# Kernel tuning notes

Measured on AMD Instinct MI355X. Metric: run time of the kernel, lower is better.

The kernel has to match this reference:

```python
import math
import jax, jax.numpy as jnp
import numpy as np

S, B, H, D = 2048, 1, 16, 128  # seq, batch, heads, head_dim (hard-coded in source)
COEFF = 1.0  # layer_num = 1
NORM_FACTOR = math.sqrt(2048 / 16) * COEFF  # sqrt(HIDDEN/NUM_HEADS) * coeff


def setup_inputs() -> dict:
    key = jax.random.key(0)
    k1, k2, k3, k4, k5 = jax.random.split(key, 5)
    query_layer = jax.random.normal(k1, (S, B, H, D), dtype=jnp.float32)
    key_layer = jax.random.normal(k2, (S, B, H, D), dtype=jnp.float32)
    value_layer = jax.random.normal(k3, (S, B, H, D), dtype=jnp.float32)
    # causal mask, True = masked (Megatron convention)
    attention_mask = jnp.triu(jnp.ones((S, S), dtype=bool), k=1)[None, None]
    # per-head SVD right-singular-vector matrices (orthonormal-ish; random here)
    svd_qk = jax.random.normal(k4, (H, D, D), dtype=jnp.float32) / math.sqrt(D)
    svd_v = jax.random.normal(k5, (H, D, D), dtype=jnp.float32) / math.sqrt(D)
    return {"query_layer": query_layer, "key_layer": key_layer,
            "value_layer": value_layer, "attention_mask": attention_mask,
            "svd_qk": svd_qk, "svd_v": svd_v}


def reference(query_layer, key_layer, value_layer, attention_mask, svd_qk, svd_v):
    # q/k/v: [S, 1, H, D] -> project each head through its SVD matrix
    q = jnp.einsum('shd,hde->hse', query_layer[:, 0], svd_qk)  # [H,S,D]
    k = jnp.einsum('shd,hde->hse', key_layer[:, 0], svd_qk)    # [H,S,D]
    # qk_drop = 0 -> h_mask zeroing of columns is a no-op (faithfully skipped)
    scores = jnp.einsum('hqe,hke->hqk', q, k) / NORM_FACTOR    # [H,S,S]
    mask = attention_mask[0, 0]                                 # [S,S] bool
    scores = jnp.where(mask, jnp.float32(-10000.0), scores)
    # FusedScaleMaskSoftmax: scale by coeff, re-mask, softmax
    scaled = jnp.where(mask, jnp.float32(-10000.0), scores * COEFF)
    probs = jax.nn.softmax(scaled, axis=-1)                     # [H,S,S]
    # attention dropout is identity in eval mode
    v = jnp.einsum('shd,hde->hse', value_layer[:, 0], svd_v)    # [H,S,D]
    # vlinear_drop = 0 -> column zeroing is a no-op
    ctx = jnp.einsum('hqk,hke->qhe', probs, v)                  # [S,H,D]
    return ctx.reshape(S, B, H * D)                             # [S,1,2048]
```

## Files before the change

### kernel.cpp

```cpp
#include <hip/hip_runtime.h>
#include <hip/hip_bf16.h>
#include <math.h>

#define S_LEN 2048
#define NHEAD 16
#define DHEAD 128

typedef __attribute__((ext_vector_type(8)))  _Float16 f16x8;
typedef __attribute__((ext_vector_type(4)))  _Float16 f16x4;
typedef __attribute__((ext_vector_type(4)))  float    f32x4;
typedef __attribute__((ext_vector_type(16))) float    f32x16;

__device__ __forceinline__ void permswap(unsigned &a, unsigned &b) {
    asm volatile("v_permlane32_swap_b32 %0, %1" : "+v"(a), "+v"(b));
}

typedef __attribute__((address_space(3))) unsigned int lds_u32;
typedef __attribute__((address_space(1))) const unsigned int glb_u32;
__device__ __forceinline__ void gload16(const void* g, void* l) {
    __builtin_amdgcn_global_load_lds((glb_u32*)g, (lds_u32*)l, 16, 0, 0);
}

__global__ __launch_bounds__(256) void transpose_w_kernel(
    const float* __restrict__ w_qk, const float* __restrict__ w_v,
    _Float16* __restrict__ wqk_t, _Float16* __restrict__ wv_t)
{
    __shared__ float tile[32][33];
    const int mat = blockIdx.z;
    const int h   = blockIdx.y;
    const int t0  = blockIdx.x;
    const int dt  = (t0 >> 2) * 32;
    const int et  = (t0 & 3) * 32;
    const float* src = (mat ? w_v : w_qk) + (size_t)h * DHEAD * DHEAD;
    _Float16*   dst = (mat ? wv_t : wqk_t) + (size_t)h * DHEAD * DHEAD;
    const int tx = threadIdx.x & 31, ty = threadIdx.x >> 5;
#pragma unroll
    for (int k = 0; k < 4; ++k)
        tile[ty + 8 * k][tx] = src[(size_t)(dt + ty + 8 * k) * DHEAD + et + tx];
    __syncthreads();
#pragma unroll
    for (int k = 0; k < 4; ++k)
        dst[(size_t)(et + ty + 8 * k) * DHEAD + dt + tx] = (_Float16)tile[tx][ty + 8 * k];
}

__global__ __launch_bounds__(256) void proj_kernel(
    const float* __restrict__ q_in, const float* __restrict__ k_in,
    const float* __restrict__ v_in,
    const _Float16* __restrict__ wqk_t, const _Float16* __restrict__ wv_t,
    _Float16* __restrict__ Qp, _Float16* __restrict__ Kp, _Float16* __restrict__ Vt)
{
    const int h   = blockIdx.x >> 5;
    const int rb  = blockIdx.x & 31;
    const int wv  = threadIdx.x >> 6;
    const int lane = threadIdx.x & 63;
    const int r16 = lane & 15;
    const int kg  = lane >> 4;
    const int s_base = rb * 64 + wv * 16;
    const int s_row  = s_base + r16;
    const float INV_NORM = 0.12752211758f;

    f16x8 aq[4], ak[4], av[4];
    {
        const float* qr = q_in + ((size_t)s_row * NHEAD + h) * DHEAD;
        const float* kr = k_in + ((size_t)s_row * NHEAD + h) * DHEAD;
        const float* vr = v_in + ((size_t)s_row * NHEAD + h) * DHEAD;
#pragma unroll
        for (int kb = 0; kb < 4; ++kb) {
            const int d0 = kb * 32 + kg * 8;
            const f32x4 q0 = *(const f32x4*)(qr + d0), q1 = *(const f32x4*)(qr + d0 + 4);
            const f32x4 k0 = *(const f32x4*)(kr + d0), k1 = *(const f32x4*)(kr + d0 + 4);
            const f32x4 v0 = *(const f32x4*)(vr + d0), v1 = *(const f32x4*)(vr + d0 + 4);
#pragma unroll
            for (int i = 0; i < 4; ++i) {
                aq[kb][i] = (_Float16)q0[i];  aq[kb][i + 4] = (_Float16)q1[i];
                ak[kb][i] = (_Float16)k0[i];  ak[kb][i + 4] = (_Float16)k1[i];
                av[kb][i] = (_Float16)v0[i];  av[kb][i + 4] = (_Float16)v1[i];
            }
        }
    }

    const _Float16* wq_h = wqk_t + (size_t)h * DHEAD * DHEAD;
    const _Float16* wv_h = wv_t  + (size_t)h * DHEAD * DHEAD;

#pragma unroll 2
    for (int cb = 0; cb < 8; ++cb) {
        f32x4 accq = {0.f, 0.f, 0.f, 0.f};
        f32x4 acck = {0.f, 0.f, 0.f, 0.f};
        f32x4 accv = {0.f, 0.f, 0.f, 0.f};
        const int c = cb * 16 + r16;
#pragma unroll
        for (int kb = 0; kb < 4; ++kb) {
            const f16x8 bqk = *(const f16x8*)(wq_h + (size_t)c * DHEAD + kb * 32 + kg * 8);
            const f16x8 bv  = *(const f16x8*)(wv_h + (size_t)c * DHEAD + kb * 32 + kg * 8);
            accq = __builtin_amdgcn_mfma_f32_16x16x32_f16(bqk, aq[kb], accq, 0, 0, 0);
            acck = __builtin_amdgcn_mfma_f32_16x16x32_f16(bqk, ak[kb], acck, 0, 0, 0);
            accv = __builtin_amdgcn_mfma_f32_16x16x32_f16(av[kb], bv,  accv, 0, 0, 0);
        }
        f16x4 qv, kv4;
#pragma unroll
        for (int jj = 0; jj < 4; ++jj) {
            qv[jj]  = (_Float16)(accq[jj] * INV_NORM);
            kv4[jj] = (_Float16)acck[jj];
        }
        *(f16x4*)(Qp + ((size_t)h * S_LEN + s_base + r16) * DHEAD + cb * 16 + kg * 4) = qv;
        *(f16x4*)(Kp + ((size_t)h * S_LEN + s_base + r16) * DHEAD + cb * 16 + kg * 4) = kv4;
        f16x4 vvv;
#pragma unroll
        for (int jj = 0; jj < 4; ++jj) vvv[jj] = (_Float16)accv[jj];
        *(f16x4*)(Vt + ((size_t)h * DHEAD + c) * S_LEN + s_base + kg * 4) = vvv;
    }
}

__device__ __forceinline__ void stage_k(const _Float16* kbase, _Float16* kst,
                                        int w, int lane, int par, int inext,
                                        int jmax_lock) {
#pragma unroll
    for (int cidx = 0; cidx < 2; ++cidx) {
        const int c      = 2 * w + cidx;
        const int role_c = c >> 3;
        const int cc     = c & 7;
        const int jn     = 2 * inext + role_c;
        if (jn < jmax_lock) {
            const int A    = cc * 1024 + lane * 16;
            const int srcO = A ^ (((A >> 8) & 15) << 4);
            const char* g  = (const char*)kbase + (size_t)jn * 8192 + srcO;
            char*       l  = (char*)kst + (size_t)(role_c * 2 + par) * 8192
                                        + cc * 1024;
            gload16(g, l);
        }
    }
}

__global__ __launch_bounds__(512, 2) void attn_kernel(
    const _Float16* __restrict__ Qp, const _Float16* __restrict__ Kp,
    const _Float16* __restrict__ Vt, float* __restrict__ out)
{
    __shared__ _Float16 Kst[4][4096];
    __shared__ _Float16 obuf[4][32][132];
    __shared__ float    mlbuf[4][2][32];

    const int h    = blockIdx.y;
    const int w    = threadIdx.x >> 6;
    const int lane = threadIdx.x & 63;
    const int q    = lane & 31;
    const int hi   = lane >> 5;

    const int qsub = w & 1;
    const int role = (w >> 1) & 1;
    const int tsel = w >> 2;
    const int t    = tsel ? (31 - blockIdx.x) : blockIdx.x;
    const int pairid = qsub + tsel * 2;
    const int q0w  = t * 64 + qsub * 32;
    const int jmax = 2 * t + 1 + qsub;
    const int q_abs = q0w + q;

    const int jmax_lock = 2 * (31 - blockIdx.x) + 2;
    const int I         = jmax_lock / 2;

    const _Float16* qbase = Qp + ((size_t)h * S_LEN + q0w) * DHEAD;
    const _Float16* kbase = Kp + (size_t)h * S_LEN * DHEAD;
    const _Float16* vbase = Vt + (size_t)h * DHEAD * S_LEN;

    const int lqk = q * DHEAD + hi * 8;
    const int lv  = q * S_LEN + hi * 8;
    const int swq = (q & 15) << 4;

    f16x8 qf[8];
#pragma unroll
    for (int m = 0; m < 8; ++m)
        qf[m] = *(const f16x8*)(qbase + lqk + m * 16);

    f32x16 acc[4];
#pragma unroll
    for (int e = 0; e < 4; ++e)
#pragma unroll
        for (int i = 0; i < 16; ++i) acc[e][i] = 0.f;

    float m_run = -1e30f, l_run = 0.f;

    stage_k(kbase, &Kst[0][0], w, lane, 0, 0, jmax_lock);

    int p = 0;
    for (int it = 0; it < I; ++it, p ^= 1) {
        __syncthreads();

        const int j   = 2 * it + role;
        const bool act = (j < jmax);
        const int kv0 = j * 32;

        f16x8 vf[8];
        if (act) {
#pragma unroll
            for (int e = 0; e < 4; ++e) {
                const _Float16* vp = vbase + (size_t)e * 32 * S_LEN + lv + kv0;
                vf[2 * e]     = *(const f16x8*)(vp);
                vf[2 * e + 1] = *(const f16x8*)(vp + 16);
            }
        }

        f16x8 kf[8];
        if (act) {
            const char* kt = (const char*)&Kst[role * 2 + p][0];
#pragma unroll
            for (int m = 0; m < 8; ++m) {
                const int L = q * 256 + m * 32 + hi * 16;
                kf[m] = *(const f16x8*)(kt + (L ^ swq));
            }
        }

        if (it + 1 < I)
            stage_k(kbase, &Kst[0][0], w, lane, p ^ 1, it + 1, jmax_lock);

        if (act) {
            f32x16 s0, s1;
#pragma unroll
            for (int i = 0; i < 16; ++i) { s0[i] = 0.f; s1[i] = 0.f; }
            __builtin_amdgcn_s_setprio(1);
#pragma unroll
            for (int m = 0; m < 8; m += 2) {
                s0 = __builtin_amdgcn_mfma_f32_32x32x16_f16(kf[m],     qf[m],     s0, 0, 0, 0);
                s1 = __builtin_amdgcn_mfma_f32_32x32x16_f16(kf[m + 1], qf[m + 1], s1, 0, 0, 0);
            }
            __builtin_amdgcn_s_setprio(0);

            f32x16 sv = s0 + s1;

            if (kv0 == q0w) {
#pragma unroll
                for (int i = 0; i < 16; ++i) {
                    const int krel = (i & 3) + 8 * (i >> 2) + 4 * hi;
                    if (kv0 + krel > q_abs) sv[i] = -1e30f;
                }
            }

            float t0 = fmaxf(sv[0], sv[1]),  t1 = fmaxf(sv[2], sv[3]);
            float t2 = fmaxf(sv[4], sv[5]),  t3 = fmaxf(sv[6], sv[7]);
            float t4 = fmaxf(sv[8], sv[9]),  t5 = fmaxf(sv[10], sv[11]);
            float t6 = fmaxf(sv[12], sv[13]), t7 = fmaxf(sv[14], sv[15]);
            t0 = fmaxf(t0, t1); t2 = fmaxf(t2, t3); t4 = fmaxf(t4, t5); t6 = fmaxf(t6, t7);
            float tm = fmaxf(fmaxf(t0, t2), fmaxf(t4, t6));
            tm = fmaxf(tm, __shfl_xor(tm, 32, 64));

            if (!__all(tm - m_run <= 8.0f)) {
                const float mnew = fmaxf(m_run, tm);
                const float corr = exp2f(m_run - mnew);
                l_run *= corr;
#pragma unroll
                for (int e = 0; e < 4; ++e)
#pragma unroll
                    for (int i = 0; i < 16; ++i) acc[e][i] *= corr;
                m_run = mnew;
            }

#pragma unroll
            for (int i = 0; i < 16; ++i) sv[i] = exp2f(sv[i] - m_run);
            float r0 = (sv[0] + sv[1]) + (sv[2] + sv[3]);
            float r1 = (sv[4] + sv[5]) + (sv[6] + sv[7]);
            float r2 = (sv[8] + sv[9]) + (sv[10] + sv[11]);
            float r3 = (sv[12] + sv[13]) + (sv[14] + sv[15]);
            float rs = (r0 + r1) + (r2 + r3);

            unsigned u0 = __builtin_bit_cast(unsigned, __builtin_amdgcn_cvt_pkrtz(sv[0],  sv[1]));
            unsigned u1 = __builtin_bit_cast(unsigned, __builtin_amdgcn_cvt_pkrtz(sv[2],  sv[3]));
            unsigned u2 = __builtin_bit_cast(unsigned, __builtin_amdgcn_cvt_pkrtz(sv[4],  sv[5]));
            unsigned u3 = __builtin_bit_cast(unsigned, __builtin_amdgcn_cvt_pkrtz(sv[6],  sv[7]));
            unsigned u4 = __builtin_bit_cast(unsigned, __builtin_amdgcn_cvt_pkrtz(sv[8],  sv[9]));
            unsigned u5 = __builtin_bit_cast(unsigned, __builtin_amdgcn_cvt_pkrtz(sv[10], sv[11]));
            unsigned u6 = __builtin_bit_cast(unsigned, __builtin_amdgcn_cvt_pkrtz(sv[12], sv[13]));
            unsigned u7 = __builtin_bit_cast(unsigned, __builtin_amdgcn_cvt_pkrtz(sv[14], sv[15]));
            permswap(u0, u2); permswap(u1, u3);
            permswap(u4, u6); permswap(u5, u7);
            union uf8 { unsigned w[4]; f16x8 v; };
            uf8 p0; p0.w[0] = u0; p0.w[1] = u1; p0.w[2] = u2; p0.w[3] = u3;
            uf8 p1; p1.w[0] = u4; p1.w[1] = u5; p1.w[2] = u6; p1.w[3] = u7;

            __builtin_amdgcn_s_setprio(1);
#pragma unroll
            for (int e = 0; e < 4; ++e) {
                acc[e] = __builtin_amdgcn_mfma_f32_32x32x16_f16(vf[2 * e],     p0.v, acc[e], 0, 0, 0);
                acc[e] = __builtin_amdgcn_mfma_f32_32x32x16_f16(vf[2 * e + 1], p1.v, acc[e], 0, 0, 0);
            }
            __builtin_amdgcn_s_setprio(0);

            rs += __shfl_xor(rs, 32, 64);
            l_run += rs;
        }
    }

    if (role) {
        if (hi == 0) { mlbuf[pairid][0][q] = m_run; mlbuf[pairid][1][q] = l_run; }
#pragma unroll
        for (int e = 0; e < 4; ++e)
#pragma unroll
            for (int i = 0; i < 16; ++i) {
                const int erow = e * 32 + (i & 3) + 8 * (i >> 2) + 4 * hi;
                obuf[pairid][q][erow] = (_Float16)acc[e][i];
            }
    }
    __syncthreads();
    if (!role) {
        const float mb = mlbuf[pairid][0][q];
        const float lb = mlbuf[pairid][1][q];
        const float ms = fmaxf(m_run, mb);
        const float ca = exp2f(m_run - ms);
        const float cb = exp2f(mb - ms);
        const float rinv = 1.0f / (l_run * ca + lb * cb);
        float* orow = out + (size_t)q_abs * (NHEAD * DHEAD) + h * DHEAD;
#pragma unroll
        for (int e = 0; e < 4; ++e) {
#pragma unroll
            for (int g = 0; g < 4; ++g) {
                f32x4 vv;
#pragma unroll
                for (int c = 0; c < 4; ++c) {
                    const int i = g * 4 + c;
                    const int erow = e * 32 + 8 * g + 4 * hi + c;
                    vv[c] = (acc[e][i] * ca + (float)obuf[pairid][q][erow] * cb) * rinv;
                }
                *(f32x4*)(orow + e * 32 + 8 * g + 4 * hi) = vv;
            }
        }
    }
}

extern "C" void kernel_launch(void* const* d_in, const int* in_sizes, int n_in,
                              void* d_out, int out_size, void* d_ws, size_t ws_size,
                              hipStream_t stream) {
    const float* q_in = (const float*)d_in[0];
    const float* k_in = (const float*)d_in[1];
    const float* v_in = (const float*)d_in[2];
    const float* w_qk = (const float*)d_in[4];
    const float* w_v  = (const float*)d_in[5];
    float* out = (float*)d_out;

    const size_t mat_elems = (size_t)NHEAD * S_LEN * DHEAD;
    const size_t w_elems   = (size_t)NHEAD * DHEAD * DHEAD;
    _Float16* Qp   = (_Float16*)d_ws;
    _Float16* Kp   = Qp + mat_elems;
    _Float16* Vt   = Kp + mat_elems;
    _Float16* Wqkt = Vt + mat_elems;
    _Float16* Wvt  = Wqkt + w_elems;

    transpose_w_kernel<<<dim3(16, NHEAD, 2), dim3(256), 0, stream>>>(w_qk, w_v, Wqkt, Wvt);
    proj_kernel<<<dim3(NHEAD * 32), dim3(256), 0, stream>>>(q_in, k_in, v_in, Wqkt, Wvt, Qp, Kp, Vt);
    attn_kernel<<<dim3(16, NHEAD), dim3(512), 0, stream>>>(Qp, Kp, Vt, out);
}
```

Before: 89.80 us.

## Split KV range four ways per query tile and process paired tiles sequentially

Each block now handles its two causal query tiles one after another, with four waves splitting the key range (4-way split-K) for each 64-row tile instead of two tiles concurrently with a 2-way split. K staging loads four key chunks per iteration into a doubled LDS buffer, and partial results are merged from three helper waves through LDS. The aim is to shorten the per-block critical path and balance work across waves, at the cost of more LDS, an extra phase barrier, and a heavier merge step.

```diff
diff --git a/kernel.cpp b/kernel.cpp
--- a/kernel.cpp
+++ b/kernel.cpp
@@ -111,20 +111,20 @@
     }
 }
 
-__device__ __forceinline__ void stage_k(const _Float16* kbase, _Float16* kst,
-                                        int w, int lane, int par, int inext,
-                                        int jmax_lock) {
-#pragma unroll
-    for (int cidx = 0; cidx < 2; ++cidx) {
-        const int c      = 2 * w + cidx;
-        const int role_c = c >> 3;
-        const int cc     = c & 7;
-        const int jn     = 2 * inext + role_c;
+__device__ __forceinline__ void stage_k4(const _Float16* kbase, _Float16* kst,
+                                         int w, int lane, int par, int inext,
+                                         int jmax_lock) {
+#pragma unroll
+    for (int cidx = 0; cidx < 4; ++cidx) {
+        const int c    = 4 * w + cidx;
+        const int slot = c >> 3;
+        const int cc   = c & 7;
+        const int jn   = 4 * inext + slot;
         if (jn < jmax_lock) {
             const int A    = cc * 1024 + lane * 16;
             const int srcO = A ^ (((A >> 8) & 15) << 4);
             const char* g  = (const char*)kbase + (size_t)jn * 8192 + srcO;
-            char*       l  = (char*)kst + (size_t)(role_c * 2 + par) * 8192
+            char*       l  = (char*)kst + (size_t)(slot * 2 + par) * 8192
                                         + cc * 1024;
             gload16(g, l);
         }
@@ -135,9 +135,9 @@
     const _Float16* __restrict__ Qp, const _Float16* __restrict__ Kp,
     const _Float16* __restrict__ Vt, float* __restrict__ out)
 {
-    __shared__ _Float16 Kst[4][4096];
-    __shared__ _Float16 obuf[4][32][132];
-    __shared__ float    mlbuf[4][2][32];
+    __shared__ _Float16 Kst[8][4096];
+    __shared__ _Float16 obuf[2][3][32][132];
+    __shared__ float    mlbuf[2][3][2][32];
 
     const int h    = blockIdx.y;
     const int w    = threadIdx.x >> 6;
@@ -145,19 +145,9 @@
     const int q    = lane & 31;
     const int hi   = lane >> 5;
 
-    const int qsub = w & 1;
-    const int role = (w >> 1) & 1;
-    const int tsel = w >> 2;
-    const int t    = tsel ? (31 - blockIdx.x) : blockIdx.x;
-    const int pairid = qsub + tsel * 2;
-    const int q0w  = t * 64 + qsub * 32;
-    const int jmax = 2 * t + 1 + qsub;
-    const int q_abs = q0w + q;
-
-    const int jmax_lock = 2 * (31 - blockIdx.x) + 2;
-    const int I         = jmax_lock / 2;
-
-    const _Float16* qbase = Qp + ((size_t)h * S_LEN + q0w) * DHEAD;
+    const int role = w & 3;
+    const int qsub = w >> 2;
+
     const _Float16* kbase = Kp + (size_t)h * S_LEN * DHEAD;
     const _Float16* vbase = Vt + (size_t)h * DHEAD * S_LEN;
 
@@ -165,159 +155,178 @@
     const int lv  = q * S_LEN + hi * 8;
     const int swq = (q & 15) << 4;
 
-    f16x8 qf[8];
-#pragma unroll
-    for (int m = 0; m < 8; ++m)
-        qf[m] = *(const f16x8*)(qbase + lqk + m * 16);
-
-    f32x16 acc[4];
-#pragma unroll
-    for (int e = 0; e < 4; ++e)
-#pragma unroll
-        for (int i = 0; i < 16; ++i) acc[e][i] = 0.f;
-
-    float m_run = -1e30f, l_run = 0.f;
-
-    stage_k(kbase, &Kst[0][0], w, lane, 0, 0, jmax_lock);
-
-    int p = 0;
-    for (int it = 0; it < I; ++it, p ^= 1) {
+    for (int ph = 0; ph < 2; ++ph) {
+        const int t     = ph ? blockIdx.x : (31 - blockIdx.x);
+        const int q0w   = t * 64 + qsub * 32;
+        const int jmax  = 2 * t + 1 + qsub;
+        const int jlock = 2 * t + 2;
+        const int I     = (jlock + 3) >> 2;
+        const int q_abs = q0w + q;
+
+        const _Float16* qbase = Qp + ((size_t)h * S_LEN + q0w) * DHEAD;
+        f16x8 qf[8];
+#pragma unroll
+        for (int m = 0; m < 8; ++m)
+            qf[m] = *(const f16x8*)(qbase + lqk + m * 16);
+
+        f32x16 acc[4];
+#pragma unroll
+        for (int e = 0; e < 4; ++e)
+#pragma unroll
+            for (int i = 0; i < 16; ++i) acc[e][i] = 0.f;
+        float m_run = -1e30f, l_run = 0.f;
+
+        stage_k4(kbase, &Kst[0][0], w, lane, 0, 0, jlock);
+
+        int p = 0;
+        for (int it = 0; it < I; ++it, p ^= 1) {
+            __syncthreads();
+
+            const int j   = 4 * it + role;
+            const bool act = (j < jmax);
+            const int kv0 = j * 32;
+
+            f16x8 vf[8];
+            if (act) {
+#pragma unroll
+                for (int e = 0; e < 4; ++e) {
+                    const _Float16* vp = vbase + (size_t)e * 32 * S_LEN + lv + kv0;
+                    vf[2 * e]     = *(const f16x8*)(vp);
+                    vf[2 * e + 1] = *(const f16x8*)(vp + 16);
+                }
+            }
+
+            f16x8 kf[8];
+            if (act) {
+                const char* kt = (const char*)&Kst[role * 2 + p][0];
+#pragma unroll
+                for (int m = 0; m < 8; ++m) {
+                    const int L = q * 256 + m * 32 + hi * 16;
+                    kf[m] = *(const f16x8*)(kt + (L ^ swq));
+                }
+            }
+
+            if (it + 1 < I)
+                stage_k4(kbase, &Kst[0][0], w, lane, p ^ 1, it + 1, jlock);
+
+            if (act) {
+                f32x16 s0, s1;
+#pragma unroll
+                for (int i = 0; i < 16; ++i) { s0[i] = 0.f; s1[i] = 0.f; }
+                __builtin_amdgcn_s_setprio(1);
+#pragma unroll
+                for (int m = 0; m < 8; m += 2) {
+                    s0 = __builtin_amdgcn_mfma_f32_32x32x16_f16(kf[m],     qf[m],     s0, 0, 0, 0);
+                    s1 = __builtin_amdgcn_mfma_f32_32x32x16_f16(kf[m + 1], qf[m + 1], s1, 0, 0, 0);
+                }
+                __builtin_amdgcn_s_setprio(0);
+
+                f32x16 sv = s0 + s1;
+
+                if (kv0 == q0w) {
+#pragma unroll
+                    for (int i = 0; i < 16; ++i) {
+                        const int krel = (i & 3) + 8 * (i >> 2) + 4 * hi;
+                        if (kv0 + krel > q_abs) sv[i] = -1e30f;
+                    }
+                }
+
+                float t0 = fmaxf(sv[0], sv[1]),  t1 = fmaxf(sv[2], sv[3]);
+                float t2 = fmaxf(sv[4], sv[5]),  t3 = fmaxf(sv[6], sv[7]);
+                float t4 = fmaxf(sv[8], sv[9]),  t5 = fmaxf(sv[10], sv[11]);
+                float t6 = fmaxf(sv[12], sv[13]), t7 = fmaxf(sv[14], sv[15]);
+                t0 = fmaxf(t0, t1); t2 = fmaxf(t2, t3);
+                t4 = fmaxf(t4, t5); t6 = fmaxf(t6, t7);
+                float tm = fmaxf(fmaxf(t0, t2), fmaxf(t4, t6));
+                tm = fmaxf(tm, __shfl_xor(tm, 32, 64));
+
+                if (!__all(tm - m_run <= 8.0f)) {
+                    const float mnew = fmaxf(m_run, tm);
+                    const float corr = exp2f(m_run - mnew);
+                    l_run *= corr;
+#pragma unroll
+                    for (int e = 0; e < 4; ++e)
+#pragma unroll
+                        for (int i = 0; i < 16; ++i) acc[e][i] *= corr;
+                    m_run = mnew;
+                }
+
+#pragma unroll
+                for (int i = 0; i < 16; ++i) sv[i] = exp2f(sv[i] - m_run);
+                float r0 = (sv[0] + sv[1]) + (sv[2] + sv[3]);
+                float r1 = (sv[4] + sv[5]) + (sv[6] + sv[7]);
+                float r2 = (sv[8] + sv[9]) + (sv[10] + sv[11]);
+                float r3 = (sv[12] + sv[13]) + (sv[14] + sv[15]);
+                float rs = (r0 + r1) + (r2 + r3);
+
+                unsigned u0 = __builtin_bit_cast(unsigned, __builtin_amdgcn_cvt_pkrtz(sv[0],  sv[1]));
+                unsigned u1 = __builtin_bit_cast(unsigned, __builtin_amdgcn_cvt_pkrtz(sv[2],  sv[3]));
+                unsigned u2 = __builtin_bit_cast(unsigned, __builtin_amdgcn_cvt_pkrtz(sv[4],  sv[5]));
+                unsigned u3 = __builtin_bit_cast(unsigned, __builtin_amdgcn_cvt_pkrtz(sv[6],  sv[7]));
+                unsigned u4 = __builtin_bit_cast(unsigned, __builtin_amdgcn_cvt_pkrtz(sv[8],  sv[9]));
+                unsigned u5 = __builtin_bit_cast(unsigned, __builtin_amdgcn_cvt_pkrtz(sv[10], sv[11]));
+                unsigned u6 = __builtin_bit_cast(unsigned, __builtin_amdgcn_cvt_pkrtz(sv[12], sv[13]));
+                unsigned u7 = __builtin_bit_cast(unsigned, __builtin_amdgcn_cvt_pkrtz(sv[14], sv[15]));
+                permswap(u0, u2); permswap(u1, u3);
+                permswap(u4, u6); permswap(u5, u7);
+                union uf8 { unsigned w[4]; f16x8 v; };
+                uf8 p0; p0.w[0] = u0; p0.w[1] = u1; p0.w[2] = u2; p0.w[3] = u3;
+                uf8 p1; p1.w[0] = u4; p1.w[1] = u5; p1.w[2] = u6; p1.w[3] = u7;
+
+                __builtin_amdgcn_s_setprio(1);
+#pragma unroll
+                for (int e = 0; e < 4; ++e) {
+                    acc[e] = __builtin_amdgcn_mfma_f32_32x32x16_f16(vf[2 * e],     p0.v, acc[e], 0, 0, 0);
+                    acc[e] = __builtin_amdgcn_mfma_f32_32x32x16_f16(vf[2 * e + 1], p1.v, acc[e], 0, 0, 0);
+                }
+                __builtin_amdgcn_s_setprio(0);
+
+                rs += __shfl_xor(rs, 32, 64);
+                l_run += rs;
+            }
+        }
+
+        if (role != 0) {
+            if (hi == 0) {
+                mlbuf[qsub][role - 1][0][q] = m_run;
+                mlbuf[qsub][role - 1][1][q] = l_run;
+            }
+#pragma unroll
+            for (int e = 0; e < 4; ++e)
+#pragma unroll
+                for (int i = 0; i < 16; ++i) {
+                    const int erow = e * 32 + (i & 3) + 8 * (i >> 2) + 4 * hi;
+                    obuf[qsub][role - 1][q][erow] = (_Float16)acc[e][i];
+                }
+        }
         __syncthreads();
-
-        const int j   = 2 * it + role;
-        const bool act = (j < jmax);
-        const int kv0 = j * 32;
-
-        f16x8 vf[8];
-        if (act) {
+        if (role == 0) {
+            const float m1 = mlbuf[qsub][0][0][q], l1 = mlbuf[qsub][0][1][q];
+            const float m2 = mlbuf[qsub][1][0][q], l2 = mlbuf[qsub][1][1][q];
+            const float m3 = mlbuf[qsub][2][0][q], l3 = mlbuf[qsub][2][1][q];
+            const float ms = fmaxf(fmaxf(m_run, m1), fmaxf(m2, m3));
+            const float c0 = exp2f(m_run - ms);
+            const float c1 = exp2f(m1 - ms);
+            const float c2 = exp2f(m2 - ms);
+            const float c3 = exp2f(m3 - ms);
+            const float rinv = 1.0f / (l_run * c0 + l1 * c1 + l2 * c2 + l3 * c3);
+            float* orow = out + (size_t)q_abs * (NHEAD * DHEAD) + h * DHEAD;
 #pragma unroll
             for (int e = 0; e < 4; ++e) {
-                const _Float16* vp = vbase + (size_t)e * 32 * S_LEN + lv + kv0;
-                vf[2 * e]     = *(const f16x8*)(vp);
-                vf[2 * e + 1] = *(const f16x8*)(vp + 16);
-            }
-        }
-
-        f16x8 kf[8];
-        if (act) {
-            const char* kt = (const char*)&Kst[role * 2 + p][0];
-#pragma unroll
-            for (int m = 0; m < 8; ++m) {
-                const int L = q * 256 + m * 32 + hi * 16;
-                kf[m] = *(const f16x8*)(kt + (L ^ swq));
-            }
-        }
-
-        if (it + 1 < I)
-            stage_k(kbase, &Kst[0][0], w, lane, p ^ 1, it + 1, jmax_lock);
-
-        if (act) {
-            f32x16 s0, s1;
-#pragma unroll
-            for (int i = 0; i < 16; ++i) { s0[i] = 0.f; s1[i] = 0.f; }
-            __builtin_amdgcn_s_setprio(1);
-#pragma unroll
-            for (int m = 0; m < 8; m += 2) {
-                s0 = __builtin_amdgcn_mfma_f32_32x32x16_f16(kf[m],     qf[m],     s0, 0, 0, 0);
-                s1 = __builtin_amdgcn_mfma_f32_32x32x16_f16(kf[m + 1], qf[m + 1], s1, 0, 0, 0);
-            }
-            __builtin_amdgcn_s_setprio(0);
-
-            f32x16 sv = s0 + s1;
-
-            if (kv0 == q0w) {
-#pragma unroll
-                for (int i = 0; i < 16; ++i) {
-                    const int krel = (i & 3) + 8 * (i >> 2) + 4 * hi;
-                    if (kv0 + krel > q_abs) sv[i] = -1e30f;
-                }
-            }
-
-            float t0 = fmaxf(sv[0], sv[1]),  t1 = fmaxf(sv[2], sv[3]);
-            float t2 = fmaxf(sv[4], sv[5]),  t3 = fmaxf(sv[6], sv[7]);
-            float t4 = fmaxf(sv[8], sv[9]),  t5 = fmaxf(sv[10], sv[11]);
-            float t6 = fmaxf(sv[12], sv[13]), t7 = fmaxf(sv[14], sv[15]);
-            t0 = fmaxf(t0, t1); t2 = fmaxf(t2, t3); t4 = fmaxf(t4, t5); t6 = fmaxf(t6, t7);
-            float tm = fmaxf(fmaxf(t0, t2), fmaxf(t4, t6));
-            tm = fmaxf(tm, __shfl_xor(tm, 32, 64));
-
-            if (!__all(tm - m_run <= 8.0f)) {
-                const float mnew = fmaxf(m_run, tm);
-                const float corr = exp2f(m_run - mnew);
-                l_run *= corr;
-#pragma unroll
-                for (int e = 0; e < 4; ++e)
-#pragma unroll
-                    for (int i = 0; i < 16; ++i) acc[e][i] *= corr;
-                m_run = mnew;
-            }
-
-#pragma unroll
-            for (int i = 0; i < 16; ++i) sv[i] = exp2f(sv[i] - m_run);
-            float r0 = (sv[0] + sv[1]) + (sv[2] + sv[3]);
-            float r1 = (sv[4] + sv[5]) + (sv[6] + sv[7]);
-            float r2 = (sv[8] + sv[9]) + (sv[10] + sv[11]);
-            float r3 = (sv[12] + sv[13]) + (sv[14] + sv[15]);
-            float rs = (r0 + r1) + (r2 + r3);
-
-            unsigned u0 = __builtin_bit_cast(unsigned, __builtin_amdgcn_cvt_pkrtz(sv[0],  sv[1]));
-            unsigned u1 = __builtin_bit_cast(unsigned, __builtin_amdgcn_cvt_pkrtz(sv[2],  sv[3]));
-            unsigned u2 = __builtin_bit_cast(unsigned, __builtin_amdgcn_cvt_pkrtz(sv[4],  sv[5]));
-            unsigned u3 = __builtin_bit_cast(unsigned, __builtin_amdgcn_cvt_pkrtz(sv[6],  sv[7]));
-            unsigned u4 = __builtin_bit_cast(unsigned, __builtin_amdgcn_cvt_pkrtz(sv[8],  sv[9]));
-            unsigned u5 = __builtin_bit_cast(unsigned, __builtin_amdgcn_cvt_pkrtz(sv[10], sv[11]));
-            unsigned u6 = __builtin_bit_cast(unsigned, __builtin_amdgcn_cvt_pkrtz(sv[12], sv[13]));
-            unsigned u7 = __builtin_bit_cast(unsigned, __builtin_amdgcn_cvt_pkrtz(sv[14], sv[15]));
-            permswap(u0, u2); permswap(u1, u3);
-            permswap(u4, u6); permswap(u5, u7);
-            union uf8 { unsigned w[4]; f16x8 v; };
-            uf8 p0; p0.w[0] = u0; p0.w[1] = u1; p0.w[2] = u2; p0.w[3] = u3;
-            uf8 p1; p1.w[0] = u4; p1.w[1] = u5; p1.w[2] = u6; p1.w[3] = u7;
-
-            __builtin_amdgcn_s_setprio(1);
-#pragma unroll
-            for (int e = 0; e < 4; ++e) {
-                acc[e] = __builtin_amdgcn_mfma_f32_32x32x16_f16(vf[2 * e],     p0.v, acc[e], 0, 0, 0);
-                acc[e] = __builtin_amdgcn_mfma_f32_32x32x16_f16(vf[2 * e + 1], p1.v, acc[e], 0, 0, 0);
-            }
-            __builtin_amdgcn_s_setprio(0);
-
-            rs += __shfl_xor(rs, 32, 64);
-            l_run += rs;
-        }
-    }
-
-    if (role) {
-        if (hi == 0) { mlbuf[pairid][0][q] = m_run; mlbuf[pairid][1][q] = l_run; }
-#pragma unroll
-        for (int e = 0; e < 4; ++e)
-#pragma unroll
-            for (int i = 0; i < 16; ++i) {
-                const int erow = e * 32 + (i & 3) + 8 * (i >> 2) + 4 * hi;
-                obuf[pairid][q][erow] = (_Float16)acc[e][i];
-            }
-    }
-    __syncthreads();
-    if (!role) {
-        const float mb = mlbuf[pairid][0][q];
-        const float lb = mlbuf[pairid][1][q];
-        const float ms = fmaxf(m_run, mb);
-        const float ca = exp2f(m_run - ms);
-        const float cb = exp2f(mb - ms);
-        const float rinv = 1.0f / (l_run * ca + lb * cb);
-        float* orow = out + (size_t)q_abs * (NHEAD * DHEAD) + h * DHEAD;
-#pragma unroll
-        for (int e = 0; e < 4; ++e) {
-#pragma unroll
-            for (int g = 0; g < 4; ++g) {
-                f32x4 vv;
-#pragma unroll
-                for (int c = 0; c < 4; ++c) {
-                    const int i = g * 4 + c;
-                    const int erow = e * 32 + 8 * g + 4 * hi + c;
-                    vv[c] = (acc[e][i] * ca + (float)obuf[pairid][q][erow] * cb) * rinv;
-                }
-                *(f32x4*)(orow + e * 32 + 8 * g + 4 * hi) = vv;
+#pragma unroll
+                for (int g = 0; g < 4; ++g) {
+                    f32x4 vv;
+#pragma unroll
+                    for (int c = 0; c < 4; ++c) {
+                        const int i = g * 4 + c;
+                        const int erow = e * 32 + 8 * g + 4 * hi + c;
+                        vv[c] = (acc[e][i] * c0
+                                 + (float)obuf[qsub][0][q][erow] * c1
+                                 + (float)obuf[qsub][1][q][erow] * c2
+                                 + (float)obuf[qsub][2][q][erow] * c3) * rinv;
+                    }
+                    *(f32x4*)(orow + e * 32 + 8 * g + 4 * hi) = vv;
+                }
             }
         }
     }
```

Measured after the change: 87.90 us. 2.1% less time.
